# Performance work log

Hardware: AMD Instinct MI355X
Metric: run time of the kernel (lower is better)

The kernel has to match this reference:

```python
import jax, jax.numpy as jnp
import numpy as np

E = 512      # room_emb_size
H = 8        # nhead
HD = E // H  # head dim
F = 32       # dim_feedforward (hardcoded in source)
L = 3        # num_layers
V = 32000    # voc_size
B = 128      # batch
T = 16       # max_sent_len == max_length
SOS = 1      # sos_idx
EPS = 1e-5   # torch LayerNorm eps


def setup_inputs() -> dict:
    key = jax.random.key(0)
    ks = jax.random.split(key, 10)
    s = 0.02
    def rn(k, shape):
        return jax.random.normal(k, shape, jnp.float32) * s
    return {
        "cur_room_emb": jax.random.normal(ks[0], (B, E), jnp.float32),
        "emb": rn(ks[1], (V, E)),
        "sa_in_w": rn(ks[2], (L, 3 * E, E)), "sa_in_b": jnp.zeros((L, 3 * E), jnp.float32),
        "sa_out_w": rn(ks[3], (L, E, E)), "sa_out_b": jnp.zeros((L, E), jnp.float32),
        "ca_in_w": rn(ks[4], (L, 3 * E, E)), "ca_in_b": jnp.zeros((L, 3 * E), jnp.float32),
        "ca_out_w": rn(ks[5], (L, E, E)), "ca_out_b": jnp.zeros((L, E), jnp.float32),
        "ff1_w": rn(ks[6], (L, F, E)), "ff1_b": jnp.zeros((L, F), jnp.float32),
        "ff2_w": rn(ks[7], (L, E, F)), "ff2_b": jnp.zeros((L, E), jnp.float32),
        "ln_g": jnp.ones((L, 3, E), jnp.float32), "ln_b": jnp.zeros((L, 3, E), jnp.float32),
        "out_w": rn(ks[8], (V, E)), "out_b": jnp.zeros((V,), jnp.float32),
        "max_length": T,
    }


def _ln(x, g, b):
    m = jnp.mean(x, axis=-1, keepdims=True)
    v = jnp.mean((x - m) ** 2, axis=-1, keepdims=True)
    return (x - m) / jnp.sqrt(v + EPS) * g + b


def _mha(qx, kvx, in_w, in_b, out_w, out_b):
    # qx: [Sq,B,E], kvx: [Sk,B,E]  (torch seq-first layout)
    wq, wk, wv = in_w[:E], in_w[E:2 * E], in_w[2 * E:]
    bq, bk, bv = in_b[:E], in_b[E:2 * E], in_b[2 * E:]
    q = (qx @ wq.T + bq).reshape(qx.shape[0], -1, H, HD)
    k = (kvx @ wk.T + bk).reshape(kvx.shape[0], -1, H, HD)
    v = (kvx @ wv.T + bv).reshape(kvx.shape[0], -1, H, HD)
    att = jax.nn.softmax(jnp.einsum('qbhd,kbhd->bhqk', q, k) / np.sqrt(HD).astype(np.float32), axis=-1)
    o = jnp.einsum('bhqk,kbhd->qbhd', att, v).reshape(qx.shape[0], -1, E)
    return o @ out_w.T + out_b


def _pos_enc(n):
    pos = np.arange(n)[:, None].astype(np.float32)
    div = np.exp(np.arange(0, E, 2).astype(np.float32) * (-np.log(10000.0) / E))
    pe = np.zeros((n, E), np.float32)
    pe[:, 0::2] = np.sin(pos * div)
    pe[:, 1::2] = np.cos(pos * div)
    return jnp.asarray(pe)


def reference(cur_room_emb, emb, sa_in_w, sa_in_b, sa_out_w, sa_out_b,
              ca_in_w, ca_in_b, ca_out_w, ca_out_b,
              ff1_w, ff1_b, ff2_w, ff2_b, ln_g, ln_b, out_w, out_b, max_length):
    pe = _pos_enc(max_length)
    bsz = cur_room_emb.shape[0]
    hx = cur_room_emb[None]  # memory [1,B,E]
    # initial <sos> embedding (no positional encoding, as in the source)
    tok_before = jnp.broadcast_to(emb[SOS][None, None, :], (1, bsz, E))
    tokens, probs_all = [], []
    for i in range(max_length):
        x = tok_before  # rerun full decoder over growing history (faithful, no KV cache)
        for l in range(L):
            x = _ln(x + _mha(x, x, sa_in_w[l], sa_in_b[l], sa_out_w[l], sa_out_b[l]), ln_g[l, 0], ln_b[l, 0])
            x = _ln(x + _mha(x, hx, ca_in_w[l], ca_in_b[l], ca_out_w[l], ca_out_b[l]), ln_g[l, 1], ln_b[l, 1])
            ff = jax.nn.relu(x @ ff1_w[l].T + ff1_b[l]) @ ff2_w[l].T + ff2_b[l]
            x = _ln(x + ff, ln_g[l, 2], ln_b[l, 2])
        probs = jax.nn.softmax(x[-1] @ out_w.T + out_b, axis=1)  # emb2idx: Linear + Softmax(dim=1)
        tok = jnp.argmax(probs, axis=1)  # greedy token choice (deterministic)
        tokens.append(tok)
        probs_all.append(probs)
        new = (emb[tok] + pe[i])[None]  # [1,B,E]: embed + positional(i)
        tok_before = jnp.concatenate([tok_before, new], axis=0)
    spoken_token = jnp.stack(tokens, axis=0).T  # [B, max_length]
    return spoken_token, jnp.stack(probs_all, axis=0)  # probs: [T,B,V]
```

## Files before the change

### kernel.cpp

```cpp
#include <hip/hip_runtime.h>
#include <math.h>

#define E   512
#define E3  1536
#define NH  8
#define FF  32
#define NL  3
#define NV  32000
#define NB  128
#define NT  16

__global__ void setup_kernel(float* __restrict__ pe, float* __restrict__ tb,
                             const float* __restrict__ emb) {
    const int bi = blockIdx.x;
    if (bi < 16) {
        for (int e = threadIdx.x; e < E; e += blockDim.x) {
            int k = e >> 1;
            double dv = exp((double)(2 * k) * (-log(10000.0) / (double)E));
            double arg = (double)bi * dv;
            pe[bi * E + e] = (e & 1) ? (float)cos(arg) : (float)sin(arg);
        }
    } else {
        const int b = bi - 16;
        for (int e = threadIdx.x; e < E; e += blockDim.x)
            tb[(size_t)b * E + e] = emb[(size_t)1 * E + e];
    }
}

__global__ __launch_bounds__(256) void ca_setup_kernel(
    const float* __restrict__ cur_room,
    const float* __restrict__ ca_in_w, const float* __restrict__ ca_in_b,
    const float* __restrict__ ca_out_w, const float* __restrict__ ca_out_b,
    float* __restrict__ ca_const)
{
    const int b = blockIdx.x, l = blockIdx.y, t = threadIdx.x;
    __shared__ float xl[E];
    __shared__ float hv[E];
    for (int e = t; e < E; e += 256) xl[e] = cur_room[(size_t)b * E + e];
    __syncthreads();
    const float* wv = ca_in_w + ((size_t)l * E3 + 2 * E) * E;
    const float* bv = ca_in_b + (size_t)l * E3 + 2 * E;
    for (int c = t; c < E; c += 256) {
        float s = bv[c];
        const float* wr = wv + (size_t)c * E;
        for (int k = 0; k < E; ++k) s += xl[k] * wr[k];
        hv[c] = s;
    }
    __syncthreads();
    const float* wo = ca_out_w + (size_t)l * E * E;
    for (int c = t; c < E; c += 256) {
        float s = ca_out_b[(size_t)l * E + c];
        const float* wr = wo + (size_t)c * E;
        for (int k = 0; k < E; ++k) s += hv[k] * wr[k];
        ca_const[((size_t)l * NB + b) * E + c] = s;
    }
}

template<bool ADD_BIAS>
__global__ __launch_bounds__(256) void gemm_v3_kernel(
    const float* __restrict__ A, const float* __restrict__ W,
    const float* __restrict__ bias, float* __restrict__ C,
    int N, int K, int KC, size_t CS, int skipm)
{
    const int m0 = blockIdx.y * 64;
    const int n0 = blockIdx.x * 128;
    if (n0 < E && m0 < skipm) return;
    __shared__ float As[16][68];
    __shared__ float Bs[16][132];
    const int tid = threadIdx.x;
    const int kc0 = blockIdx.z * KC;
    const int tx = tid & 15;
    const int ty = tid >> 4;
    const int sr = tid >> 2;
    const int sc = (tid & 3) * 4;

    const float* Ap  = A + (size_t)(m0 + sr) * K + kc0 + sc;
    const float* Wp0 = W + (size_t)(n0 + sr) * K + kc0 + sc;
    const float* Wp1 = W + (size_t)(n0 + 64 + sr) * K + kc0 + sc;

    float4 pa  = *(const float4*)Ap;
    float4 pb0 = *(const float4*)Wp0;
    float4 pb1 = *(const float4*)Wp1;

    float acc[4][8] = {};
    const int nkt = KC >> 4;
    for (int kt = 0; kt < nkt; ++kt) {
        __syncthreads();
        As[sc + 0][sr] = pa.x;  As[sc + 1][sr] = pa.y;
        As[sc + 2][sr] = pa.z;  As[sc + 3][sr] = pa.w;
        Bs[sc + 0][sr] = pb0.x; Bs[sc + 1][sr] = pb0.y;
        Bs[sc + 2][sr] = pb0.z; Bs[sc + 3][sr] = pb0.w;
        Bs[sc + 0][64 + sr] = pb1.x; Bs[sc + 1][64 + sr] = pb1.y;
        Bs[sc + 2][64 + sr] = pb1.z; Bs[sc + 3][64 + sr] = pb1.w;
        __syncthreads();
        if (kt + 1 < nkt) {
            const int off = 16 * (kt + 1);
            pa  = *(const float4*)(Ap + off);
            pb0 = *(const float4*)(Wp0 + off);
            pb1 = *(const float4*)(Wp1 + off);
        }
#pragma unroll
        for (int k = 0; k < 16; ++k) {
            float a[4], b[8];
            *(float4*)&a[0] = *(const float4*)&As[k][ty * 4];
            *(float4*)&b[0] = *(const float4*)&Bs[k][tx * 4];
            *(float4*)&b[4] = *(const float4*)&Bs[k][64 + tx * 4];
#pragma unroll
            for (int i = 0; i < 4; ++i)
#pragma unroll
                for (int j = 0; j < 8; ++j)
                    acc[i][j] += a[i] * b[j];
        }
    }
    float* Co = C + (size_t)blockIdx.z * CS;
#pragma unroll
    for (int i = 0; i < 4; ++i) {
        const int m = m0 + ty * 4 + i;
#pragma unroll
        for (int cj = 0; cj < 2; ++cj) {
            const int n = n0 + cj * 64 + tx * 4;
            float4 o;
            o.x = acc[i][cj * 4 + 0];
            o.y = acc[i][cj * 4 + 1];
            o.z = acc[i][cj * 4 + 2];
            o.w = acc[i][cj * 4 + 3];
            if (ADD_BIAS) {
                const float4 bv = *(const float4*)&bias[n];
                o.x += bv.x; o.y += bv.y; o.z += bv.z; o.w += bv.w;
            }
            *(float4*)&Co[(size_t)m * N + n] = o;
        }
    }
}

__global__ __launch_bounds__(256) void gemm_v4_kernel(
    const float* __restrict__ A, const float* __restrict__ W,
    float* __restrict__ C, int N, int K, int KC, size_t CS, int skipm)
{
    const int n0 = blockIdx.x * 128;
    const int m0 = blockIdx.y * 128;
    if (n0 < E && m0 < skipm) return;
    __shared__ float As[16][132];
    __shared__ float Bs[16][132];
    const int tid = threadIdx.x;
    const int kc0 = blockIdx.z * KC;
    const int tx = tid & 15, ty = tid >> 4;
    const int sr = tid >> 1;
    const int sc = (tid & 1) * 8;

    const float* Ap = A + (size_t)(m0 + sr) * K + kc0 + sc;
    const float* Wp = W + (size_t)(n0 + sr) * K + kc0 + sc;
    float4 pa0 = *(const float4*)Ap;
    float4 pa1 = *(const float4*)(Ap + 4);
    float4 pb0 = *(const float4*)Wp;
    float4 pb1 = *(const float4*)(Wp + 4);

    float acc[8][8] = {};
    const int nkt = KC >> 4;
    for (int kt = 0; kt < nkt; ++kt) {
        __syncthreads();
        As[sc + 0][sr] = pa0.x; As[sc + 1][sr] = pa0.y; As[sc + 2][sr] = pa0.z; As[sc + 3][sr] = pa0.w;
        As[sc + 4][sr] = pa1.x; As[sc + 5][sr] = pa1.y; As[sc + 6][sr] = pa1.z; As[sc + 7][sr] = pa1.w;
        Bs[sc + 0][sr] = pb0.x; Bs[sc + 1][sr] = pb0.y; Bs[sc + 2][sr] = pb0.z; Bs[sc + 3][sr] = pb0.w;
        Bs[sc + 4][sr] = pb1.x; Bs[sc + 5][sr] = pb1.y; Bs[sc + 6][sr] = pb1.z; Bs[sc + 7][sr] = pb1.w;
        __syncthreads();
        if (kt + 1 < nkt) {
            const int off = 16 * (kt + 1);
            pa0 = *(const float4*)(Ap + off);
            pa1 = *(const float4*)(Ap + off + 4);
            pb0 = *(const float4*)(Wp + off);
            pb1 = *(const float4*)(Wp + off + 4);
        }
#pragma unroll
        for (int k = 0; k < 16; ++k) {
            float a[8], b[8];
            *(float4*)&a[0] = *(const float4*)&As[k][ty * 4];
            *(float4*)&a[4] = *(const float4*)&As[k][64 + ty * 4];
            *(float4*)&b[0] = *(const float4*)&Bs[k][tx * 4];
            *(float4*)&b[4] = *(const float4*)&Bs[k][64 + tx * 4];
#pragma unroll
            for (int i = 0; i < 8; ++i)
#pragma unroll
                for (int jj = 0; jj < 8; ++jj)
                    acc[i][jj] += a[i] * b[jj];
        }
    }
    float* Co = C + (size_t)blockIdx.z * CS;
#pragma unroll
    for (int ih = 0; ih < 2; ++ih)
#pragma unroll
        for (int i = 0; i < 4; ++i) {
            const int m = m0 + ih * 64 + ty * 4 + i;
#pragma unroll
            for (int jh = 0; jh < 2; ++jh) {
                const int n = n0 + jh * 64 + tx * 4;
                float4 o;
                o.x = acc[ih * 4 + i][jh * 4 + 0];
                o.y = acc[ih * 4 + i][jh * 4 + 1];
                o.z = acc[ih * 4 + i][jh * 4 + 2];
                o.w = acc[ih * 4 + i][jh * 4 + 3];
                *(float4*)&Co[(size_t)m * N + n] = o;
            }
        }
}

template<bool WB>
__global__ __launch_bounds__(128) void attn_kernel(
    const float* __restrict__ qkv, size_t QS, int pcount,
    const float* __restrict__ cache, float* __restrict__ wbdst,
    const float* __restrict__ bias,
    float* __restrict__ o, int S, int qstart)
{
    const int b = blockIdx.x >> 3;
    const int h = blockIdx.x & 7;
    __shared__ float Ks[16][64];
    __shared__ float Vs[16][64];
    const int tid = threadIdx.x;
    if (WB) {
        for (int e = tid; e < 192; e += 128) {
            const int part = e >> 6, d = e & 63;
            const int go = part * E + h * 64 + d;
            float v = 0.f;
#pragma unroll
            for (int p = 0; p < 8; ++p) v += qkv[(size_t)p * QS + (size_t)b * E3 + go];
            wbdst[(size_t)b * E3 + go] = v;
            if (part == 1) Ks[S - 1][d] = v + bias[go];
            else if (part == 2) Vs[S - 1][d] = v + bias[go];
        }
        for (int idx = tid; idx < (S - 1) * 64; idx += 128) {
            const int s = idx >> 6, d = idx & 63;
            const size_t base = ((size_t)(s * NB + b)) * E3 + h * 64 + d;
            Ks[s][d] = cache[base + E] + bias[E + h * 64 + d];
            Vs[s][d] = cache[base + 2 * E] + bias[2 * E + h * 64 + d];
        }
    } else {
        for (int idx = tid; idx < S * 64; idx += 128) {
            const int s = idx >> 6, d = idx & 63;
            const size_t base = ((size_t)(s * NB + b)) * E3 + h * 64 + d;
            float kk = bias[E + h * 64 + d];
            float vv = bias[2 * E + h * 64 + d];
            for (int p = 0; p < pcount; ++p) {
                kk += qkv[(size_t)p * QS + base + E];
                vv += qkv[(size_t)p * QS + base + 2 * E];
            }
            Ks[s][d] = kk;
            Vs[s][d] = vv;
        }
    }
    __syncthreads();
    const int wid = tid >> 6, lane = tid & 63;
    const float bq = bias[h * 64 + lane];
    for (int qi = qstart + wid; qi < S; qi += 2) {
        const size_t qbase = ((size_t)(qi * NB + b)) * E3 + h * 64 + lane;
        float qd = bq;
        if (WB) qd += cache[qbase];
        else for (int p = 0; p < pcount; ++p) qd += qkv[(size_t)p * QS + qbase];
        float sc[16];
#pragma unroll
        for (int ki = 0; ki < 16; ++ki) {
            float p = 0.f;
            if (ki < S) {
                p = qd * Ks[ki][lane];
#pragma unroll
                for (int off = 32; off; off >>= 1) p += __shfl_xor(p, off);
                p *= 0.125f;
            }
            sc[ki] = p;
        }
        float m = -1e30f;
#pragma unroll
        for (int ki = 0; ki < 16; ++ki) if (ki < S) m = fmaxf(m, sc[ki]);
        float sum = 0.f;
#pragma unroll
        for (int ki = 0; ki < 16; ++ki) if (ki < S) { sc[ki] = expf(sc[ki] - m); sum += sc[ki]; }
        float inv = 1.0f / sum;
        float acc = 0.f;
#pragma unroll
        for (int ki = 0; ki < 16; ++ki) if (ki < S) acc += sc[ki] * Vs[ki][lane];
        o[((size_t)(qi * NB + b)) * E + h * 64 + lane] = acc * inv;
    }
}

__global__ __launch_bounds__(256) void epilogue_kernel(
    const float* __restrict__ xin,
    const float* __restrict__ yp, size_t YS, int pcount,
    const float* __restrict__ ob,
    const float* __restrict__ ca,
    const float* __restrict__ g0, const float* __restrict__ b0,
    const float* __restrict__ g1, const float* __restrict__ b1,
    const float* __restrict__ w1, const float* __restrict__ b1f,
    const float* __restrict__ w2, const float* __restrict__ b2f,
    const float* __restrict__ g2, const float* __restrict__ bb2,
    float* __restrict__ xout, int rows)
{
    const int wid = threadIdx.x >> 6, lane = threadIdx.x & 63;
    const int row = blockIdx.x * 4 + wid;
    if (row >= rows) return;
    const float* xr = xin + (size_t)row * E;
    const float* cr = ca + (size_t)(row & (NB - 1)) * E;
    float v[8];
    float s = 0.f;
#pragma unroll
    for (int j = 0; j < 8; ++j) {
        int e = j * 64 + lane;
        float y = xr[e] + ob[e];
        for (int p = 0; p < pcount; ++p) y += yp[(size_t)p * YS + (size_t)row * E + e];
        v[j] = y; s += y;
    }
#pragma unroll
    for (int off = 32; off; off >>= 1) s += __shfl_xor(s, off);
    float mean = s * (1.0f / E);
    float vs = 0.f;
#pragma unroll
    for (int j = 0; j < 8; ++j) { float d = v[j] - mean; vs += d * d; }
#pragma unroll
    for (int off = 32; off; off >>= 1) vs += __shfl_xor(vs, off);
    float rstd = rsqrtf(vs * (1.0f / E) + 1e-5f);
#pragma unroll
    for (int j = 0; j < 8; ++j) {
        int e = j * 64 + lane;
        v[j] = (v[j] - mean) * rstd * g0[e] + b0[e] + cr[e];
    }
    s = 0.f;
#pragma unroll
    for (int j = 0; j < 8; ++j) s += v[j];
#pragma unroll
    for (int off = 32; off; off >>= 1) s += __shfl_xor(s, off);
    mean = s * (1.0f / E);
    vs = 0.f;
#pragma unroll
    for (int j = 0; j < 8; ++j) { float d = v[j] - mean; vs += d * d; }
#pragma unroll
    for (int off = 32; off; off >>= 1) vs += __shfl_xor(vs, off);
    rstd = rsqrtf(vs * (1.0f / E) + 1e-5f);
#pragma unroll
    for (int j = 0; j < 8; ++j) {
        int e = j * 64 + lane;
        v[j] = (v[j] - mean) * rstd * g1[e] + b1[e];
    }
    float h[FF];
#pragma unroll
    for (int f = 0; f < FF; ++f) {
        float p = 0.f;
#pragma unroll
        for (int j = 0; j < 8; ++j) p += v[j] * w1[(size_t)f * E + j * 64 + lane];
#pragma unroll
        for (int off = 32; off; off >>= 1) p += __shfl_xor(p, off);
        h[f] = fmaxf(p + b1f[f], 0.f);
    }
    float o[8];
#pragma unroll
    for (int j = 0; j < 8; ++j) {
        int e = j * 64 + lane;
        float acc = b2f[e];
#pragma unroll
        for (int f4 = 0; f4 < FF / 4; ++f4) {
            float4 w4 = *(const float4*)&w2[(size_t)e * FF + f4 * 4];
            acc += h[f4 * 4 + 0] * w4.x + h[f4 * 4 + 1] * w4.y +
                   h[f4 * 4 + 2] * w4.z + h[f4 * 4 + 3] * w4.w;
        }
        o[j] = v[j] + acc;
    }
    s = 0.f;
#pragma unroll
    for (int j = 0; j < 8; ++j) s += o[j];
#pragma unroll
    for (int off = 32; off; off >>= 1) s += __shfl_xor(s, off);
    mean = s * (1.0f / E);
    vs = 0.f;
#pragma unroll
    for (int j = 0; j < 8; ++j) { float d = o[j] - mean; vs += d * d; }
#pragma unroll
    for (int off = 32; off; off >>= 1) vs += __shfl_xor(vs, off);
    rstd = rsqrtf(vs * (1.0f / E) + 1e-5f);
#pragma unroll
    for (int j = 0; j < 8; ++j) {
        int e = j * 64 + lane;
        xout[(size_t)row * E + e] = (o[j] - mean) * rstd * g2[e] + bb2[e];
    }
}

__global__ __launch_bounds__(1024) void softmax_v2_kernel(
    const float* __restrict__ p0, const float* __restrict__ p1,
    const float* __restrict__ ob,
    float* __restrict__ probs_out, float* __restrict__ tok_out,
    const float* __restrict__ emb, const float* __restrict__ pe_row,
    float* __restrict__ tb_new, int step)
{
    const int b = blockIdx.x, t = threadIdx.x;
    const float* q0 = p0 + (size_t)b * NV;
    const float* q1 = p1 + (size_t)b * NV;
    float r[32];
    float vmax = -1e30f; int imax = 0x7fffffff;
#pragma unroll
    for (int j = 0; j < 32; ++j) {
        const int idx = j * 1024 + t;
        if (idx < NV) {
            const float v = ob[idx] + q0[idx] + q1[idx];
            r[j] = v;
            if (v > vmax) { vmax = v; imax = idx; }
        } else r[j] = -1e30f;
    }
    const int wid = t >> 6, lane = t & 63;
#pragma unroll
    for (int off = 32; off; off >>= 1) {
        const float ov = __shfl_xor(vmax, off);
        const int oi = __shfl_xor(imax, off);
        if (ov > vmax || (ov == vmax && oi < imax)) { vmax = ov; imax = oi; }
    }
    __shared__ float swv[16]; __shared__ int swi[16]; __shared__ float ssum[16];
    __shared__ float sbc[2];
    if (lane == 0) { swv[wid] = vmax; swi[wid] = imax; }
    __syncthreads();
    if (wid == 0) {
        float v = (lane < 16) ? swv[lane] : -1e30f;
        int ii = (lane < 16) ? swi[lane] : 0x7fffffff;
#pragma unroll
        for (int off = 8; off; off >>= 1) {
            const float ov = __shfl_xor(v, off);
            const int oi = __shfl_xor(ii, off);
            if (ov > v || (ov == v && oi < ii)) { v = ov; ii = oi; }
        }
        if (lane == 0) { sbc[0] = v; swi[0] = ii; }
    }
    __syncthreads();
    const float m = sbc[0];
    const int tok = swi[0];
    float psum = 0.f;
#pragma unroll
    for (int j = 0; j < 32; ++j) {
        const int idx = j * 1024 + t;
        if (idx < NV) { r[j] = expf(r[j] - m); psum += r[j]; }
    }
#pragma unroll
    for (int off = 32; off; off >>= 1) psum += __shfl_xor(psum, off);
    if (lane == 0) ssum[wid] = psum;
    __syncthreads();
    if (t == 0) {
        float s = 0.f;
        for (int ww = 0; ww < 16; ++ww) s += ssum[ww];
        sbc[1] = 1.0f / s;
    }
    __syncthreads();
    const float inv = sbc[1];
    float* P = probs_out + (size_t)b * NV;
#pragma unroll
    for (int j = 0; j < 32; ++j) {
        const int idx = j * 1024 + t;
        if (idx < NV) P[idx] = r[j] * inv;
    }
    if (t == 0) tok_out[(size_t)b * NT + step] = (float)tok;
    if (t < E) tb_new[(size_t)b * E + t] = emb[(size_t)tok * E + t] + pe_row[t];
}

extern "C" void kernel_launch(void* const* d_in, const int* in_sizes, int n_in,
                              void* d_out, int out_size, void* d_ws, size_t ws_size,
                              hipStream_t stream) {
    const float* cur_room = (const float*)d_in[0];
    const float* emb      = (const float*)d_in[1];
    const float* sa_in_w  = (const float*)d_in[2];
    const float* sa_in_b  = (const float*)d_in[3];
    const float* sa_out_w = (const float*)d_in[4];
    const float* sa_out_b = (const float*)d_in[5];
    const float* ca_in_w  = (const float*)d_in[6];
    const float* ca_in_b  = (const float*)d_in[7];
    const float* ca_out_w = (const float*)d_in[8];
    const float* ca_out_b = (const float*)d_in[9];
    const float* ff1_w    = (const float*)d_in[10];
    const float* ff1_b    = (const float*)d_in[11];
    const float* ff2_w    = (const float*)d_in[12];
    const float* ff2_b    = (const float*)d_in[13];
    const float* ln_g     = (const float*)d_in[14];
    const float* ln_b     = (const float*)d_in[15];
    const float* out_w    = (const float*)d_in[16];
    const float* out_b    = (const float*)d_in[17];
    float* out = (float*)d_out;

    float* ws = (float*)d_ws;
    float* pe       = ws;
    float* ca_const = pe + 16 * E;
    float* tokb     = ca_const + (size_t)NL * NB * E;
    float* x        = tokb + (size_t)17 * NB * E;
    float* qkv0p    = x + (size_t)NT * NB * E;
    float* qkv0     = qkv0p + (size_t)8 * NB * E3;
    float* qkvp     = qkv0 + (size_t)NT * NB * E3;
    float* attn_o   = qkvp + (size_t)32 * NB * E3;
    float* ypart    = attn_o + (size_t)NT * NB * E;
    float* vocp     = ypart + (size_t)8 * NT * NB * E;

    setup_kernel<<<144, 256, 0, stream>>>(pe, tokb, emb);
    ca_setup_kernel<<<dim3(NB, NL), 256, 0, stream>>>(
        cur_room, ca_in_w, ca_in_b, ca_out_w, ca_out_b, ca_const);

    const size_t QS0 = (size_t)NB * E3;

    for (int i = 0; i < NT; ++i) {
        const int S = i + 1;
        const int M = S * NB;
        const size_t QSM = (size_t)M * E3;
        const size_t YSM = (size_t)M * E;

        gemm_v3_kernel<false><<<dim3(E3 / 128, 2, 8), 256, 0, stream>>>(
            tokb + (size_t)i * NB * E, sa_in_w, nullptr, qkv0p, E3, E, 64, QS0, 0);

        const int z_out = (S <= 4) ? 8 : 4;
        for (int l = 0; l < NL; ++l) {
            const float* xin = (l == 0) ? tokb : x;
            const int skipm = (l == 2) ? (S - 1) * NB : 0;
            const int qstart = (l == 2) ? S - 1 : 0;

            if (l == 0) {
                attn_kernel<true><<<NB * NH, 128, 0, stream>>>(
                    qkv0p, QS0, 8, qkv0, qkv0 + (size_t)i * NB * E3,
                    sa_in_b, attn_o, S, 0);
            } else {
                const int z = (S <= 2) ? 8 : (S <= 6) ? 4 : 2;
                gemm_v3_kernel<false><<<dim3(E3 / 128, 2 * S, z), 256, 0, stream>>>(
                    x, sa_in_w + (size_t)l * E3 * E, nullptr, qkvp, E3, E, E / z, QSM, skipm);
                attn_kernel<false><<<NB * NH, 128, 0, stream>>>(
                    qkvp, QSM, z, nullptr, nullptr,
                    sa_in_b + (size_t)l * E3, attn_o, S, qstart);
            }

            if (l == 2) {
                gemm_v3_kernel<false><<<dim3(E / 128, 2, 8), 256, 0, stream>>>(
                    attn_o + (size_t)(S - 1) * NB * E, sa_out_w + (size_t)l * E * E,
                    nullptr, ypart, E, E, 64, (size_t)NB * E, 0);
                epilogue_kernel<<<32, 256, 0, stream>>>(
                    xin + (size_t)(S - 1) * NB * E, ypart, (size_t)NB * E, 8,
                    sa_out_b + (size_t)l * E, ca_const + (size_t)l * NB * E,
                    ln_g + (size_t)(l * 3 + 0) * E, ln_b + (size_t)(l * 3 + 0) * E,
                    ln_g + (size_t)(l * 3 + 1) * E, ln_b + (size_t)(l * 3 + 1) * E,
                    ff1_w + (size_t)l * FF * E, ff1_b + (size_t)l * FF,
                    ff2_w + (size_t)l * E * FF, ff2_b + (size_t)l * E,
                    ln_g + (size_t)(l * 3 + 2) * E, ln_b + (size_t)(l * 3 + 2) * E,
                    x + (size_t)(S - 1) * NB * E, NB);
            } else {
                gemm_v3_kernel<false><<<dim3(E / 128, 2 * S, z_out), 256, 0, stream>>>(
                    attn_o, sa_out_w + (size_t)l * E * E, nullptr,
                    ypart, E, E, E / z_out, YSM, 0);
                epilogue_kernel<<<S * 32, 256, 0, stream>>>(
                    xin, ypart, YSM, z_out,
                    sa_out_b + (size_t)l * E, ca_const + (size_t)l * NB * E,
                    ln_g + (size_t)(l * 3 + 0) * E, ln_b + (size_t)(l * 3 + 0) * E,
                    ln_g + (size_t)(l * 3 + 1) * E, ln_b + (size_t)(l * 3 + 1) * E,
                    ff1_w + (size_t)l * FF * E, ff1_b + (size_t)l * FF,
                    ff2_w + (size_t)l * E * FF, ff2_b + (size_t)l * E,
                    ln_g + (size_t)(l * 3 + 2) * E, ln_b + (size_t)(l * 3 + 2) * E,
                    x, M);
            }
        }
        gemm_v4_kernel<<<dim3(NV / 128, 1, 2), 256, 0, stream>>>(
            x + (size_t)i * NB * E, out_w, vocp, NV, E, 256, (size_t)NB * NV, 0);
        softmax_v2_kernel<<<NB, 1024, 0, stream>>>(
            vocp, vocp + (size_t)NB * NV, out_b,
            out + 2048 + (size_t)i * NB * NV, out,
            emb, pe + (size_t)i * E, tokb + (size_t)S * NB * E, i);
    }
}
```

Before: 5.372 ms.

## Compute vocab projection with bf16 MFMA and rescore top candidates in fp32

```diff
diff --git a/kernel.cpp b/kernel.cpp
--- a/kernel.cpp
+++ b/kernel.cpp
@@ -1,4 +1,5 @@
 #include <hip/hip_runtime.h>
+#include <hip/hip_bf16.h>
 #include <math.h>
 
 #define E   512
@@ -9,6 +10,10 @@
 #define NV  32000
 #define NB  128
 #define NT  16
+#define RESCUE_DELTA 0.08f
+
+typedef __attribute__((ext_vector_type(8))) short bf16x8;
+typedef __attribute__((ext_vector_type(4))) float f32x4;
 
 __global__ void setup_kernel(float* __restrict__ pe, float* __restrict__ tb,
                              const float* __restrict__ emb) {
@@ -25,6 +30,21 @@
         for (int e = threadIdx.x; e < E; e += blockDim.x)
             tb[(size_t)b * E + e] = emb[(size_t)1 * E + e];
     }
+}
+
+__global__ __launch_bounds__(256) void cvt_bf16_kernel(
+    const float* __restrict__ src, unsigned short* __restrict__ dst)
+{
+    const int i = (blockIdx.x * 256 + threadIdx.x) * 4;
+    const float4 v = *(const float4*)&src[i];
+    __hip_bfloat16 h0 = __float2bfloat16(v.x);
+    __hip_bfloat16 h1 = __float2bfloat16(v.y);
+    __hip_bfloat16 h2 = __float2bfloat16(v.z);
+    __hip_bfloat16 h3 = __float2bfloat16(v.w);
+    dst[i + 0] = *(unsigned short*)&h0;
+    dst[i + 1] = *(unsigned short*)&h1;
+    dst[i + 2] = *(unsigned short*)&h2;
+    dst[i + 3] = *(unsigned short*)&h3;
 }
 
 __global__ __launch_bounds__(256) void ca_setup_kernel(
@@ -133,75 +153,46 @@
     }
 }
 
-__global__ __launch_bounds__(256) void gemm_v4_kernel(
-    const float* __restrict__ A, const float* __restrict__ W,
-    float* __restrict__ C, int N, int K, int KC, size_t CS, int skipm)
-{
-    const int n0 = blockIdx.x * 128;
-    const int m0 = blockIdx.y * 128;
-    if (n0 < E && m0 < skipm) return;
-    __shared__ float As[16][132];
-    __shared__ float Bs[16][132];
-    const int tid = threadIdx.x;
-    const int kc0 = blockIdx.z * KC;
-    const int tx = tid & 15, ty = tid >> 4;
-    const int sr = tid >> 1;
-    const int sc = (tid & 1) * 8;
-
-    const float* Ap = A + (size_t)(m0 + sr) * K + kc0 + sc;
-    const float* Wp = W + (size_t)(n0 + sr) * K + kc0 + sc;
-    float4 pa0 = *(const float4*)Ap;
-    float4 pa1 = *(const float4*)(Ap + 4);
-    float4 pb0 = *(const float4*)Wp;
-    float4 pb1 = *(const float4*)(Wp + 4);
-
-    float acc[8][8] = {};
-    const int nkt = KC >> 4;
-    for (int kt = 0; kt < nkt; ++kt) {
-        __syncthreads();
-        As[sc + 0][sr] = pa0.x; As[sc + 1][sr] = pa0.y; As[sc + 2][sr] = pa0.z; As[sc + 3][sr] = pa0.w;
-        As[sc + 4][sr] = pa1.x; As[sc + 5][sr] = pa1.y; As[sc + 6][sr] = pa1.z; As[sc + 7][sr] = pa1.w;
-        Bs[sc + 0][sr] = pb0.x; Bs[sc + 1][sr] = pb0.y; Bs[sc + 2][sr] = pb0.z; Bs[sc + 3][sr] = pb0.w;
-        Bs[sc + 4][sr] = pb1.x; Bs[sc + 5][sr] = pb1.y; Bs[sc + 6][sr] = pb1.z; Bs[sc + 7][sr] = pb1.w;
-        __syncthreads();
-        if (kt + 1 < nkt) {
-            const int off = 16 * (kt + 1);
-            pa0 = *(const float4*)(Ap + off);
-            pa1 = *(const float4*)(Ap + off + 4);
-            pb0 = *(const float4*)(Wp + off);
-            pb1 = *(const float4*)(Wp + off + 4);
-        }
-#pragma unroll
-        for (int k = 0; k < 16; ++k) {
-            float a[8], b[8];
-            *(float4*)&a[0] = *(const float4*)&As[k][ty * 4];
-            *(float4*)&a[4] = *(const float4*)&As[k][64 + ty * 4];
-            *(float4*)&b[0] = *(const float4*)&Bs[k][tx * 4];
-            *(float4*)&b[4] = *(const float4*)&Bs[k][64 + tx * 4];
-#pragma unroll
-            for (int i = 0; i < 8; ++i)
-#pragma unroll
-                for (int jj = 0; jj < 8; ++jj)
-                    acc[i][jj] += a[i] * b[jj];
-        }
-    }
-    float* Co = C + (size_t)blockIdx.z * CS;
-#pragma unroll
-    for (int ih = 0; ih < 2; ++ih)
-#pragma unroll
-        for (int i = 0; i < 4; ++i) {
-            const int m = m0 + ih * 64 + ty * 4 + i;
-#pragma unroll
-            for (int jh = 0; jh < 2; ++jh) {
-                const int n = n0 + jh * 64 + tx * 4;
-                float4 o;
-                o.x = acc[ih * 4 + i][jh * 4 + 0];
-                o.y = acc[ih * 4 + i][jh * 4 + 1];
-                o.z = acc[ih * 4 + i][jh * 4 + 2];
-                o.w = acc[ih * 4 + i][jh * 4 + 3];
-                *(float4*)&Co[(size_t)m * N + n] = o;
-            }
-        }
+__global__ __launch_bounds__(256) void vgemm_bf16_kernel(
+    const unsigned short* __restrict__ Abf,
+    const unsigned short* __restrict__ Wbf,
+    const float* __restrict__ bias, float* __restrict__ Cout)
+{
+    const int wid = threadIdx.x >> 6, lane = threadIdx.x & 63;
+    const int n0 = (blockIdx.x * 4 + wid) * 32;
+    const int r = lane & 15;
+    const int ko = (lane >> 4) * 8;
+    f32x4 acc[2][8];
+#pragma unroll
+    for (int nt = 0; nt < 2; ++nt)
+#pragma unroll
+        for (int m = 0; m < 8; ++m)
+            acc[nt][m] = (f32x4){0.f, 0.f, 0.f, 0.f};
+
+    const unsigned short* a0 = Abf + (size_t)r * E + ko;
+    const unsigned short* w0 = Wbf + (size_t)(n0 + r) * E + ko;
+    const unsigned short* w1 = Wbf + (size_t)(n0 + 16 + r) * E + ko;
+    for (int k0 = 0; k0 < E; k0 += 32) {
+        const bf16x8 b0 = *(const bf16x8*)(w0 + k0);
+        const bf16x8 b1 = *(const bf16x8*)(w1 + k0);
+#pragma unroll
+        for (int m = 0; m < 8; ++m) {
+            const bf16x8 af = *(const bf16x8*)(a0 + (size_t)m * 16 * E + k0);
+            acc[0][m] = __builtin_amdgcn_mfma_f32_16x16x32_bf16(af, b0, acc[0][m], 0, 0, 0);
+            acc[1][m] = __builtin_amdgcn_mfma_f32_16x16x32_bf16(af, b1, acc[1][m], 0, 0, 0);
+        }
+    }
+    const int crow = (lane >> 4) * 4;
+#pragma unroll
+    for (int nt = 0; nt < 2; ++nt) {
+        const int col = n0 + nt * 16 + r;
+        const float bv = bias[col];
+#pragma unroll
+        for (int m = 0; m < 8; ++m)
+#pragma unroll
+            for (int rr = 0; rr < 4; ++rr)
+                Cout[(size_t)(m * 16 + crow + rr) * NV + col] = acc[nt][m][rr] + bv;
+    }
 }
 
 template<bool WB>
@@ -291,7 +282,7 @@
     const float* __restrict__ w1, const float* __restrict__ b1f,
     const float* __restrict__ w2, const float* __restrict__ b2f,
     const float* __restrict__ g2, const float* __restrict__ bb2,
-    float* __restrict__ xout, int rows)
+    float* __restrict__ xout, unsigned short* __restrict__ xbf, int rows)
 {
     const int wid = threadIdx.x >> 6, lane = threadIdx.x & 63;
     const int row = blockIdx.x * 4 + wid;
@@ -376,56 +367,86 @@
 #pragma unroll
     for (int j = 0; j < 8; ++j) {
         int e = j * 64 + lane;
-        xout[(size_t)row * E + e] = (o[j] - mean) * rstd * g2[e] + bb2[e];
-    }
-}
-
-__global__ __launch_bounds__(1024) void softmax_v2_kernel(
-    const float* __restrict__ p0, const float* __restrict__ p1,
+        const float val = (o[j] - mean) * rstd * g2[e] + bb2[e];
+        xout[(size_t)row * E + e] = val;
+        if (xbf) {
+            __hip_bfloat16 hb = __float2bfloat16(val);
+            xbf[(size_t)row * E + e] = *(unsigned short*)&hb;
+        }
+    }
+}
+
+__global__ __launch_bounds__(1024) void softmax_v3_kernel(
+    const float* __restrict__ logits,
+    const float* __restrict__ xrow,
+    const float* __restrict__ out_w,
     const float* __restrict__ ob,
     float* __restrict__ probs_out, float* __restrict__ tok_out,
     const float* __restrict__ emb, const float* __restrict__ pe_row,
     float* __restrict__ tb_new, int step)
 {
     const int b = blockIdx.x, t = threadIdx.x;
-    const float* q0 = p0 + (size_t)b * NV;
-    const float* q1 = p1 + (size_t)b * NV;
+    const int wid = t >> 6, lane = t & 63;
+    const float* L = logits + (size_t)b * NV;
     float r[32];
-    float vmax = -1e30f; int imax = 0x7fffffff;
+    float vmax = -1e30f;
 #pragma unroll
     for (int j = 0; j < 32; ++j) {
         const int idx = j * 1024 + t;
-        if (idx < NV) {
-            const float v = ob[idx] + q0[idx] + q1[idx];
-            r[j] = v;
-            if (v > vmax) { vmax = v; imax = idx; }
-        } else r[j] = -1e30f;
-    }
-    const int wid = t >> 6, lane = t & 63;
-#pragma unroll
-    for (int off = 32; off; off >>= 1) {
-        const float ov = __shfl_xor(vmax, off);
-        const int oi = __shfl_xor(imax, off);
-        if (ov > vmax || (ov == vmax && oi < imax)) { vmax = ov; imax = oi; }
-    }
-    __shared__ float swv[16]; __shared__ int swi[16]; __shared__ float ssum[16];
+        if (idx < NV) { r[j] = L[idx]; vmax = fmaxf(vmax, r[j]); }
+        else r[j] = -1e30f;
+    }
+#pragma unroll
+    for (int off = 32; off; off >>= 1) vmax = fmaxf(vmax, __shfl_xor(vmax, off));
+    __shared__ float swv[16];
+    __shared__ float ssum[16];
     __shared__ float sbc[2];
-    if (lane == 0) { swv[wid] = vmax; swi[wid] = imax; }
-    __syncthreads();
-    if (wid == 0) {
-        float v = (lane < 16) ? swv[lane] : -1e30f;
-        int ii = (lane < 16) ? swi[lane] : 0x7fffffff;
-#pragma unroll
-        for (int off = 8; off; off >>= 1) {
-            const float ov = __shfl_xor(v, off);
-            const int oi = __shfl_xor(ii, off);
-            if (ov > v || (ov == v && oi < ii)) { v = ov; ii = oi; }
-        }
-        if (lane == 0) { sbc[0] = v; swi[0] = ii; }
+    __shared__ int scnt;
+    __shared__ int cand[64];
+    __shared__ float cex[64];
+    __shared__ int stok;
+    if (lane == 0) swv[wid] = vmax;
+    if (t == 0) scnt = 0;
+    __syncthreads();
+    if (t == 0) {
+        float m = swv[0];
+        for (int w = 1; w < 16; ++w) m = fmaxf(m, swv[w]);
+        sbc[0] = m;
     }
     __syncthreads();
     const float m = sbc[0];
-    const int tok = swi[0];
+#pragma unroll
+    for (int j = 0; j < 32; ++j) {
+        const int idx = j * 1024 + t;
+        if (idx < NV && r[j] >= m - RESCUE_DELTA) {
+            const int p = atomicAdd(&scnt, 1);
+            if (p < 64) cand[p] = idx;
+        }
+    }
+    __syncthreads();
+    const int nc = min(scnt, 64);
+    const float* xr = xrow + (size_t)b * E;
+    for (int c = wid; c < nc; c += 16) {
+        const float* wr = out_w + (size_t)cand[c] * E;
+        const float4 a0 = *(const float4*)&xr[lane * 8];
+        const float4 a1 = *(const float4*)&xr[lane * 8 + 4];
+        const float4 w0 = *(const float4*)&wr[lane * 8];
+        const float4 w1 = *(const float4*)&wr[lane * 8 + 4];
+        float s = a0.x * w0.x + a0.y * w0.y + a0.z * w0.z + a0.w * w0.w +
+                  a1.x * w1.x + a1.y * w1.y + a1.z * w1.z + a1.w * w1.w;
+#pragma unroll
+        for (int off = 32; off; off >>= 1) s += __shfl_xor(s, off);
+        if (lane == 0) cex[c] = s + ob[cand[c]];
+    }
+    __syncthreads();
+    if (t == 0) {
+        float bv = -1e30f; int bi = 0x7fffffff;
+        for (int c = 0; c < nc; ++c) {
+            const float v = cex[c]; const int ii = cand[c];
+            if (v > bv || (v == bv && ii < bi)) { bv = v; bi = ii; }
+        }
+        stok = bi;
+    }
     float psum = 0.f;
 #pragma unroll
     for (int j = 0; j < 32; ++j) {
@@ -438,11 +459,12 @@
     __syncthreads();
     if (t == 0) {
         float s = 0.f;
-        for (int ww = 0; ww < 16; ++ww) s += ssum[ww];
+        for (int w = 0; w < 16; ++w) s += ssum[w];
         sbc[1] = 1.0f / s;
     }
     __syncthreads();
     const float inv = sbc[1];
+    const int tok = stok;
     float* P = probs_out + (size_t)b * NV;
 #pragma unroll
     for (int j = 0; j < 32; ++j) {
@@ -486,11 +508,14 @@
     float* qkvp     = qkv0 + (size_t)NT * NB * E3;
     float* attn_o   = qkvp + (size_t)32 * NB * E3;
     float* ypart    = attn_o + (size_t)NT * NB * E;
-    float* vocp     = ypart + (size_t)8 * NT * NB * E;
+    float* vocp     = ypart + (size_t)4718592;
+    unsigned short* wbf = (unsigned short*)(vocp + (size_t)NB * NV);
+    unsigned short* xbf = wbf + (size_t)NV * E;
 
     setup_kernel<<<144, 256, 0, stream>>>(pe, tokb, emb);
     ca_setup_kernel<<<dim3(NB, NL), 256, 0, stream>>>(
         cur_room, ca_in_w, ca_in_b, ca_out_w, ca_out_b, ca_const);
+    cvt_bf16_kernel<<<(NV * E) / 1024, 256, 0, stream>>>(out_w, wbf);
 
     const size_t QS0 = (size_t)NB * E3;
 
@@ -534,7 +559,7 @@
                     ff1_w + (size_t)l * FF * E, ff1_b + (size_t)l * FF,
                     ff2_w + (size_t)l * E * FF, ff2_b + (size_t)l * E,
                     ln_g + (size_t)(l * 3 + 2) * E, ln_b + (size_t)(l * 3 + 2) * E,
-                    x + (size_t)(S - 1) * NB * E, NB);
+                    x + (size_t)(S - 1) * NB * E, xbf, NB);
             } else {
                 gemm_v3_kernel<false><<<dim3(E / 128, 2 * S, z_out), 256, 0, stream>>>(
                     attn_o, sa_out_w + (size_t)l * E * E, nullptr,
@@ -547,13 +572,12 @@
                     ff1_w + (size_t)l * FF * E, ff1_b + (size_t)l * FF,
                     ff2_w + (size_t)l * E * FF, ff2_b + (size_t)l * E,
                     ln_g + (size_t)(l * 3 + 2) * E, ln_b + (size_t)(l * 3 + 2) * E,
-                    x, M);
+                    x, nullptr, M);
             }
         }
-        gemm_v4_kernel<<<dim3(NV / 128, 1, 2), 256, 0, stream>>>(
-            x + (size_t)i * NB * E, out_w, vocp, NV, E, 256, (size_t)NB * NV, 0);
-        softmax_v2_kernel<<<NB, 1024, 0, stream>>>(
-            vocp, vocp + (size_t)NB * NV, out_b,
+        vgemm_bf16_kernel<<<NV / 128, 256, 0, stream>>>(xbf, wbf, out_b, vocp);
+        softmax_v3_kernel<<<NB, 1024, 0, stream>>>(
+            vocp, x + (size_t)i * NB * E, out_w, out_b,
             out + 2048 + (size_t)i * NB * NV, out,
             emb, pe + (size_t)i * E, tokb + (size_t)S * NB * E, i);
     }
```

New measurement: 4.940 ms. 8.0% less time.
